# Kernel tuning notes

Measured on AMD Instinct MI355X. Metric: run time of the kernel, lower is better.

The kernel has to match this reference:

```python
import jax, jax.numpy as jnp
import numpy as np

N, E, B = 100000, 400000, 4096      # nodes, directed edges, graphs
P, d = 4, 49                        # phm_dim, per-component dim; D = P*d = 196
L = 3                               # message-passing layers
D1, D2 = 64, 32                     # downstream per-component dims (256/4, 128/4)


def setup_inputs():
    key = jax.random.key(0)
    ks = jax.random.split(key, 20)
    def nrm(k, shape, s=0.1):
        return jax.random.normal(k, shape, dtype=jnp.float32) * s
    return {
        "x": jax.random.randint(ks[0], (N, 9), 0, 119),
        "edge_index": jax.random.randint(ks[1], (2, E), 0, N),
        "edge_attr": jax.random.randint(ks[2], (E, 3), 0, 8),
        "batch": jnp.sort(jax.random.randint(ks[3], (N,), 0, B)),
        # encoders: summed categorical embeddings in hypercomplex form [*, P, d]
        "atom_emb": nrm(ks[4], (9, 119, P, d)),
        "bond_emb": nrm(ks[5], (L, 3, 8, P, d)),
        # per-layer PHM conv: contribution matrices A (phm rule) + component weights W
        "conv_A": nrm(ks[6], (L, P, P, P), 0.5),
        "conv_W": nrm(ks[7], (L, P, d, d)),
        "conv_b": jnp.zeros((L, P, d), jnp.float32),
        "mp_gamma": jnp.ones((L, P * d), jnp.float32),
        "mp_beta": jnp.zeros((L, P * d), jnp.float32),
        # soft-attention pooling: PHM linear + real transformer gate
        "pool_A": nrm(ks[8], (P, P, P), 0.5),
        "pool_W": nrm(ks[9], (P, d, d)),
        "pool_b": jnp.zeros((P, d), jnp.float32),
        "pool_rt_w": nrm(ks[10], (P,), 0.5),
        "pool_rt_b": jnp.zeros((d,), jnp.float32),
        # downstream PHM MLP 196 -> 256 -> 128 -> 4*1, then real trafo -> 1
        "dn_A": nrm(ks[11], (3, P, P, P), 0.5),
        "dn1_W": nrm(ks[12], (P, d, D1)),
        "dn1_b": jnp.zeros((P, D1), jnp.float32),
        "dn1_gamma": jnp.ones((P * D1,), jnp.float32),
        "dn1_beta": jnp.zeros((P * D1,), jnp.float32),
        "dn2_W": nrm(ks[13], (P, D1, D2)),
        "dn2_b": jnp.zeros((P, D2), jnp.float32),
        "dn2_gamma": jnp.ones((P * D2,), jnp.float32),
        "dn2_beta": jnp.zeros((P * D2,), jnp.float32),
        "dn3_W": nrm(ks[14], (P, D2, 1)),
        "dn3_b": jnp.zeros((P, 1), jnp.float32),
        "rt_w": nrm(ks[15], (P,), 0.5),
        "rt_b": jnp.zeros((1,), jnp.float32),
    }


def phm_linear(x, A, W, b):
    # PHM linear: y = x @ (sum_i kron(A_i, W_i)) + b, on [n, P, din] -> [n, P, dout]
    return jnp.einsum('nkp,ikj,ipq->njq', x, A, W) + b


def naive_bn(x, gamma, beta, eps=1e-5):
    # naive batch norm over the batch axis, per flattened hypercomplex feature
    n, p, dd = x.shape
    x2 = x.reshape(n, p * dd)
    mu = x2.mean(axis=0)
    var = x2.var(axis=0)
    x2 = (x2 - mu) * jax.lax.rsqrt(var + eps) * gamma + beta
    return x2.reshape(n, p, dd)


def reference(x, edge_index, edge_attr, batch, atom_emb, bond_emb,
              conv_A, conv_W, conv_b, mp_gamma, mp_beta,
              pool_A, pool_W, pool_b, pool_rt_w, pool_rt_b,
              dn_A, dn1_W, dn1_b, dn1_gamma, dn1_beta,
              dn2_W, dn2_b, dn2_gamma, dn2_beta, dn3_W, dn3_b, rt_w, rt_b):
    src, dst = edge_index[0], edge_index[1]
    # atom encoder: sum embeddings of 9 categorical features -> [N, P, d]
    h0 = atom_emb[jnp.arange(9), x].sum(axis=1)
    h = h0
    for l in range(L):  # small fixed layer count
        # bond encoder for this layer -> [E, P, d]
        e = bond_emb[l][jnp.arange(3), edge_attr].sum(axis=1)
        # message = x_j + e_ij (identity msg encoder); self-loop (zero edge feat) adds h
        m = h[src] + e
        agg = jax.ops.segment_sum(m, dst, num_segments=N) + h
        z = phm_linear(agg, conv_A[l], conv_W[l], conv_b[l])
        z = jax.nn.relu(naive_bn(z, mp_gamma[l], mp_beta[l]))
        h = z + h0  # skip-connect to first embedding (sc_type='first')
    # soft-attention pooling: real-valued sigmoid gate per node feature
    g = jax.nn.sigmoid(
        jnp.einsum('npk,p->nk', phm_linear(h, pool_A, pool_W, pool_b), pool_rt_w)
        + pool_rt_b)
    pooled = jax.ops.segment_sum(h * g[:, None, :], batch, num_segments=B)  # [B, P, d]
    # downstream PHM MLP with naive batch norm + relu
    z = jax.nn.relu(naive_bn(phm_linear(pooled, dn_A[0], dn1_W, dn1_b), dn1_gamma, dn1_beta))
    z = jax.nn.relu(naive_bn(phm_linear(z, dn_A[1], dn2_W, dn2_b), dn2_gamma, dn2_beta))
    o = phm_linear(z, dn_A[2], dn3_W, dn3_b)          # [B, P, 1]
    return jnp.einsum('npk,p->nk', o, rt_w) + rt_b    # [B, 1]
```

## Files before the change

kernel.cpp:

```cpp
#include <hip/hip_runtime.h>
#include <cstdint>
#include <cstddef>

#define N_NODES 100000
#define N_EDGES 400000
#define N_GRAPHS 4096
#define DF 196
#define DD 49
#define NPB 5
#define TST 200
#define WSLOT 14336
#define EST 232

typedef __bf16 bf16x8 __attribute__((ext_vector_type(8)));
typedef float f32x4 __attribute__((ext_vector_type(4)));

__device__ __forceinline__ unsigned short f2bf(float f) {
  unsigned int u = __float_as_uint(f);
  u = u + 0x7FFFu + ((u >> 16) & 1u);
  return (unsigned short)(u >> 16);
}
__device__ __forceinline__ float bf2f(unsigned short h) {
  return __uint_as_float(((unsigned int)h) << 16);
}

__global__ void convert_wfrag_kernel(const float* __restrict__ cA,
                                     const float* __restrict__ cW,
                                     unsigned short* __restrict__ wfrag) {
  int idx = blockIdx.x * blockDim.x + threadIdx.x;
  if (idx >= 3 * 100352) return;
  int l = idx / 100352;
  int r = idx - l * 100352;
  int ct = r / 7168; int r1 = r - ct * 7168;
  int ks = r1 / 1024; int r2 = r1 - ks * 1024;
  int h = r2 / 512;  int r3 = r2 - h * 512;
  int ln = r3 / 8;   int j = r3 - ln * 8;
  int col = ct * 16 + (ln & 15);
  int k = ks * 32 + (ln >> 4) * 8 + j;
  float v = 0.f;
  if (col < DF && k < DF) {
    int k4 = k / DD, p = k - (k / DD) * DD;
    int j4 = col / DD, q = col - (col / DD) * DD;
#pragma unroll
    for (int i = 0; i < 4; i++)
      v += cA[((l * 4 + i) * 4 + k4) * 4 + j4] * cW[((l * 4 + i) * DD + p) * DD + q];
  }
  unsigned short hi = f2bf(v);
  wfrag[idx] = (h == 0) ? hi : f2bf(v - bf2f(hi));
}

__global__ void setup_small_kernel(const float* __restrict__ bond, float* __restrict__ lut,
                                   const float* __restrict__ pA, const float* __restrict__ pW,
                                   const float* __restrict__ pb, const float* __restrict__ rtw,
                                   const float* __restrict__ rtb,
                                   float* __restrict__ gateW, float* __restrict__ gbias,
                                   const float* __restrict__ dnA,
                                   const float* __restrict__ W1, const float* __restrict__ W2,
                                   const float* __restrict__ W3,
                                   float* __restrict__ M1, float* __restrict__ M2,
                                   float* __restrict__ M3) {
  int idx0 = blockIdx.x * blockDim.x + threadIdx.x;
  const int NL = 3 * 512 * DF;
  const int NG = DF * DD + DD;
  const int n1 = DF * 256, n2 = 256 * 128, n3 = 128 * 4;
  if (idx0 < NL) {
    int idx = idx0;
    int l = idx / (512 * DF);
    int r = idx - l * (512 * DF);
    int code = r / DF, c = r - (r / DF) * DF;
    int a0 = code & 7, a1 = (code >> 3) & 7, a2 = (code >> 6) & 7;
    lut[idx] = bond[((l * 3 + 0) * 8 + a0) * DF + c]
             + bond[((l * 3 + 1) * 8 + a1) * DF + c]
             + bond[((l * 3 + 2) * 8 + a2) * DF + c];
  } else if (idx0 < NL + NG) {
    int idx = idx0 - NL;
    if (idx < DF * DD) {
      int r = idx / DD, q = idx - (idx / DD) * DD;
      int k = r / DD, p = r - (r / DD) * DD;
      float s = 0.f;
#pragma unroll
      for (int i = 0; i < 4; i++) {
        float aw = 0.f;
#pragma unroll
        for (int j = 0; j < 4; j++) aw += pA[(i * 4 + k) * 4 + j] * rtw[j];
        s += aw * pW[(i * DD + p) * DD + q];
      }
      gateW[idx] = s;
    } else {
      int q = idx - DF * DD;
      float s = rtb[q];
#pragma unroll
      for (int j = 0; j < 4; j++) s += rtw[j] * pb[j * DD + q];
      gbias[q] = s;
    }
  } else if (idx0 < NL + NG + n1 + n2 + n3) {
    int idx = idx0 - NL - NG;
    if (idx < n1) {
      int r = idx >> 8, c = idx & 255;
      int k = r / DD, p = r - (r / DD) * DD;
      int j = c >> 6, Q = c & 63;
      float s = 0.f;
#pragma unroll
      for (int i = 0; i < 4; i++) s += dnA[i * 16 + k * 4 + j] * W1[(i * DD + p) * 64 + Q];
      M1[idx] = s;
    } else if (idx < n1 + n2) {
      int m = idx - n1;
      int r = m >> 7, c = m & 127;
      int k = r >> 6, p = r & 63, j = c >> 5, q = c & 31;
      float s = 0.f;
#pragma unroll
      for (int i = 0; i < 4; i++) s += dnA[64 + i * 16 + k * 4 + j] * W2[(i * 64 + p) * 32 + q];
      M2[m] = s;
    } else {
      int m = idx - n1 - n2;
      int r = m >> 2, j = m & 3;
      int k = r >> 5, p = r & 31;
      float s = 0.f;
#pragma unroll
      for (int i = 0; i < 4; i++) s += dnA[128 + i * 16 + k * 4 + j] * W3[i * 32 + p];
      M3[m] = s;
    }
  }
}

__global__ void hist_kernel(const int* __restrict__ dst, int* __restrict__ counts) {
  int e = blockIdx.x * blockDim.x + threadIdx.x;
  if (e < N_EDGES) atomicAdd(&counts[dst[e]], 1);
}

__global__ void scan_local_kernel(const int* __restrict__ counts, int* __restrict__ offs,
                                  int* __restrict__ bsum) {
  __shared__ int sm[256];
  int tid = threadIdx.x;
  int gid = blockIdx.x * 256 + tid;
  int v = (gid < N_NODES) ? counts[gid] : 0;
  sm[tid] = v;
  __syncthreads();
  for (int d = 1; d < 256; d <<= 1) {
    int add = (tid >= d) ? sm[tid - d] : 0;
    __syncthreads();
    sm[tid] += add;
    __syncthreads();
  }
  if (gid < N_NODES) offs[gid] = sm[tid] - v;
  if (tid == 255) bsum[blockIdx.x] = sm[255];
}

__global__ void scan_bsum_kernel(int* __restrict__ bsum, int* __restrict__ bpre, int nb) {
  __shared__ int sm[512];
  int tid = threadIdx.x;
  int v = (tid < nb) ? bsum[tid] : 0;
  sm[tid] = v;
  __syncthreads();
  for (int d = 1; d < 512; d <<= 1) {
    int add = (tid >= d) ? sm[tid - d] : 0;
    __syncthreads();
    sm[tid] += add;
    __syncthreads();
  }
  if (tid < nb) bpre[tid] = sm[tid] - v;
}

__global__ void add_off_kernel(int* __restrict__ offs, const int* __restrict__ bpre) {
  int gid = blockIdx.x * blockDim.x + threadIdx.x;
  if (gid < N_NODES) offs[gid] += bpre[gid >> 8];
  if (gid == 0) offs[N_NODES] = N_EDGES;
}

__global__ void scatter_kernel(const int* __restrict__ src, const int* __restrict__ dst,
                               const int* __restrict__ ea, int* __restrict__ counts,
                               const int* __restrict__ offs,
                               unsigned int* __restrict__ sorted) {
  int e = blockIdx.x * blockDim.x + threadIdx.x;
  if (e >= N_EDGES) return;
  int d = dst[e];
  int code = ea[e * 3 + 0] | (ea[e * 3 + 1] << 3) | (ea[e * 3 + 2] << 6);
  int pos = offs[d] + atomicSub(&counts[d], 1) - 1;
  sorted[pos] = (unsigned int)src[e] | ((unsigned int)code << 17);
}

__global__ void sortseg_kernel(const int* __restrict__ offs,
                               unsigned int* __restrict__ sorted) {
  int n = blockIdx.x * blockDim.x + threadIdx.x;
  if (n >= N_NODES) return;
  int s = offs[n], e = offs[n + 1];
  for (int i = s + 1; i < e; i++) {
    unsigned int v = sorted[i];
    int j = i - 1;
    while (j >= s && sorted[j] > v) { sorted[j + 1] = sorted[j]; j--; }
    sorted[j + 1] = v;
  }
}

__global__ void atom_enc_kernel(const int* __restrict__ x, const float* __restrict__ emb,
                                float* __restrict__ h0) {
  int idx = blockIdx.x * blockDim.x + threadIdx.x;
  if (idx >= N_NODES * DF) return;
  int n = idx / DF;
  int c = idx - n * DF;
  float s = 0.f;
#pragma unroll
  for (int f = 0; f < 9; f++) {
    int xi = x[n * 9 + f];
    s += emb[(f * 119 + xi) * DF + c];
  }
  h0[idx] = s;
}

__global__ __launch_bounds__(256)
void agg_kernel(const float* __restrict__ h, const int* __restrict__ offs,
                const unsigned int* __restrict__ sorted, const float* __restrict__ lut,
                unsigned short* __restrict__ tH, unsigned short* __restrict__ tL) {
  int t = threadIdx.x;
  int i = t / 49, q = t - i * 49;
  if (i >= NPB) return;
  int node = blockIdx.x * NPB + i;
  if (node >= N_NODES) return;
  const float4* h4 = (const float4*)h;
  const float4* l4 = (const float4*)lut;
  float4 acc = h4[(size_t)node * 49 + q];
  int s = offs[node], e = offs[node + 1];
  for (int k = s; k < e; k++) {
    unsigned int se = sorted[k];
    int srcn = se & 0x1FFFF;
    int code = se >> 17;
    float4 hv = h4[(size_t)srcn * 49 + q];
    float4 lv = l4[(size_t)code * 49 + q];
    acc.x += hv.x + lv.x;
    acc.y += hv.y + lv.y;
    acc.z += hv.z + lv.z;
    acc.w += hv.w + lv.w;
  }
  ushort4 hh, ll;
  hh.x = f2bf(acc.x); ll.x = f2bf(acc.x - bf2f(hh.x));
  hh.y = f2bf(acc.y); ll.y = f2bf(acc.y - bf2f(hh.y));
  hh.z = f2bf(acc.z); ll.z = f2bf(acc.z - bf2f(hh.z));
  hh.w = f2bf(acc.w); ll.w = f2bf(acc.w - bf2f(hh.w));
  size_t ob = (size_t)node * TST + q * 4;
  *(ushort4*)(tH + ob) = hh;
  *(ushort4*)(tL + ob) = ll;
  if (q == 48) {
    ushort4 z = make_ushort4(0, 0, 0, 0);
    *(ushort4*)(tH + (size_t)node * TST + 196) = z;
    *(ushort4*)(tL + (size_t)node * TST + 196) = z;
  }
}

__global__ __launch_bounds__(256, 2)
void conv_mfma_kernel(unsigned short* __restrict__ tH,
                      unsigned short* __restrict__ tL,
                      const unsigned short* __restrict__ wfrag,
                      const float* __restrict__ bias,
                      float* __restrict__ stats) {
  __shared__ __align__(16) unsigned short smW[2 * 64 * EST];
  const int t = threadIdx.x;
  const int lane = t & 63;
  const int w = t >> 6;
  const int li = lane & 15;
  const int rg = lane >> 4;
  const int rowbase = blockIdx.x * 128 + w * 32;

  f32x4 acc[2][14];
#pragma unroll
  for (int rt = 0; rt < 2; rt++)
#pragma unroll
    for (int ct = 0; ct < 14; ct++) acc[rt][ct] = (f32x4){0.f, 0.f, 0.f, 0.f};

  uint4 b0h[2], b0l[2], b1h[2], b1l[2], b2h[2], b2l[2];
  uint4 wr0[7], wr1[7];

#define LOADA(ks, aH, aL)                                                      \
  {                                                                            \
    _Pragma("unroll") for (int rt = 0; rt < 2; rt++) {                         \
      size_t o = (size_t)(rowbase + rt * 16 + li) * TST + (ks) * 32 + rg * 8;  \
      aH[rt] = *(const uint4*)(tH + o);                                        \
      aL[rt] = *(const uint4*)(tL + o);                                        \
    }                                                                          \
  }

#define GLOADW(ks, wr)                                                         \
  {                                                                            \
    _Pragma("unroll") for (int f0 = 0; f0 < 7; f0++) {                         \
      int f = f0 * 256 + t;                                                    \
      int ln = f & 63, g = f >> 6;                                             \
      int hh = g & 1, ct = g >> 1;                                             \
      wr[f0] = *(const uint4*)(wfrag +                                         \
          (((size_t)(ct * 7 + (ks)) * 2 + hh) * 512 + ln * 8));                \
    }                                                                          \
  }

#define DSWRITEW(wr, sbase)                                                    \
  {                                                                            \
    _Pragma("unroll") for (int f0 = 0; f0 < 7; f0++) {                         \
      int f = f0 * 256 + t;                                                    \
      int ln = f & 63, g = f >> 6;                                             \
      int hh = g & 1, ct = g >> 1;                                             \
      *(uint4*)(smW + (sbase) + ((ct * 2 + hh) * 512 + ln * 8)) = wr[f0];      \
    }                                                                          \
  }

#define COMPUTE(sbase, aH, aL)                                                 \
  {                                                                            \
    _Pragma("unroll") for (int ct = 0; ct < 14; ct++) {                        \
      bf16x8 bh = *(const bf16x8*)(smW + (sbase) + ((ct * 2 + 0) * 512 + lane * 8)); \
      bf16x8 bl = *(const bf16x8*)(smW + (sbase) + ((ct * 2 + 1) * 512 + lane * 8)); \
      _Pragma("unroll") for (int rt = 0; rt < 2; rt++) {                       \
        bf16x8 ah = *(const bf16x8*)&aH[rt];                                   \
        bf16x8 al = *(const bf16x8*)&aL[rt];                                   \
        acc[rt][ct] = __builtin_amdgcn_mfma_f32_16x16x32_bf16(ah, bh, acc[rt][ct], 0, 0, 0); \
        acc[rt][ct] = __builtin_amdgcn_mfma_f32_16x16x32_bf16(al, bh, acc[rt][ct], 0, 0, 0); \
        acc[rt][ct] = __builtin_amdgcn_mfma_f32_16x16x32_bf16(ah, bl, acc[rt][ct], 0, 0, 0); \
      }                                                                        \
    }                                                                          \
  }

  GLOADW(0, wr0);
  GLOADW(1, wr1);
  LOADA(0, b0h, b0l);
  LOADA(1, b1h, b1l);
  LOADA(2, b2h, b2l);
  DSWRITEW(wr0, 0);
  GLOADW(2, wr0);
  __syncthreads();
  COMPUTE(0, b0h, b0l);
  DSWRITEW(wr1, WSLOT);
  GLOADW(3, wr1);
  LOADA(3, b0h, b0l);
  __syncthreads();
  COMPUTE(WSLOT, b1h, b1l);
  DSWRITEW(wr0, 0);
  GLOADW(4, wr0);
  LOADA(4, b1h, b1l);
  __syncthreads();
  COMPUTE(0, b2h, b2l);
  DSWRITEW(wr1, WSLOT);
  GLOADW(5, wr1);
  LOADA(5, b2h, b2l);
  __syncthreads();
  COMPUTE(WSLOT, b0h, b0l);
  DSWRITEW(wr0, 0);
  GLOADW(6, wr0);
  LOADA(6, b0h, b0l);
  __syncthreads();
  COMPUTE(0, b1h, b1l);
  DSWRITEW(wr1, WSLOT);
  __syncthreads();
  COMPUTE(WSLOT, b2h, b2l);
  DSWRITEW(wr0, 0);
  __syncthreads();
  COMPUTE(0, b0h, b0l);

  float part[14], psq[14];
#pragma unroll
  for (int ct = 0; ct < 14; ct++) { part[ct] = 0.f; psq[ct] = 0.f; }

  unsigned short* lhi = smW;
  unsigned short* llo = smW + 64 * EST;

#pragma unroll
  for (int half = 0; half < 2; half++) {
    __syncthreads();
    if ((w >> 1) == half) {
      int rl0 = (w & 1) * 32;
#pragma unroll
      for (int ct = 0; ct < 14; ct++) {
        int c = ct * 16 + li;
        float bv = (c < DF) ? bias[c] : 0.f;
#pragma unroll
        for (int rt = 0; rt < 2; rt++) {
#pragma unroll
          for (int r = 0; r < 4; r++) {
            int row = rl0 + rt * 16 + rg * 4 + r;
            int gr = rowbase + rt * 16 + rg * 4 + r;
            float y = acc[rt][ct][r] + bv;
            if (gr < N_NODES && c < DF) { part[ct] += y; psq[ct] += y * y; }
            unsigned short hi = f2bf(y);
            lhi[row * EST + c] = hi;
            llo[row * EST + c] = f2bf(y - bf2f(hi));
          }
        }
      }
    }
    __syncthreads();
    for (int idx = t; idx < 1600; idx += 256) {
      int row = idx / 25, u = idx - (idx / 25) * 25;
      int gr = blockIdx.x * 128 + half * 64 + row;
      if (gr < N_NODES) {
        uint4 vh = *(const uint4*)(lhi + row * EST + u * 8);
        uint4 vl = *(const uint4*)(llo + row * EST + u * 8);
        if (u == 24) { vh.z = 0u; vh.w = 0u; vl.z = 0u; vl.w = 0u; }
        *(uint4*)(tH + (size_t)gr * TST + u * 8) = vh;
        *(uint4*)(tL + (size_t)gr * TST + u * 8) = vl;
      }
    }
  }

  __syncthreads();
  float* redS = (float*)smW;
  float* redQ = redS + 4 * 224;
#pragma unroll
  for (int ct = 0; ct < 14; ct++) {
    float p = part[ct], q = psq[ct];
    p += __shfl_xor(p, 16, 64); p += __shfl_xor(p, 32, 64);
    q += __shfl_xor(q, 16, 64); q += __shfl_xor(q, 32, 64);
    if (rg == 0) { redS[w * 224 + ct * 16 + li] = p; redQ[w * 224 + ct * 16 + li] = q; }
  }
  __syncthreads();
  if (t < DF) {
    float s1 = redS[t] + redS[224 + t] + redS[448 + t] + redS[672 + t];
    float s2 = redQ[t] + redQ[224 + t] + redQ[448 + t] + redQ[672 + t];
    atomicAdd(&stats[t], s1);
    atomicAdd(&stats[DF + t], s2);
  }
#undef LOADA
#undef GLOADW
#undef DSWRITEW
#undef COMPUTE
}

__global__ void bn_relu_split_kernel(const unsigned short* __restrict__ tH,
                                     const unsigned short* __restrict__ tL,
                                     const float* __restrict__ stats,
                                     const float* __restrict__ gamma,
                                     const float* __restrict__ beta,
                                     const float* __restrict__ h0,
                                     float* __restrict__ h) {
  int idx = blockIdx.x * blockDim.x + threadIdx.x;
  if (idx >= N_NODES * DD) return;
  int n = idx / DD, q = idx - (idx / DD) * DD;
  size_t ib = (size_t)n * TST + q * 4;
  ushort4 hv = *(const ushort4*)(tH + ib);
  ushort4 lv = *(const ushort4*)(tL + ib);
  size_t fb = (size_t)n * DF + q * 4;
  float4 sk = *(const float4*)(h0 + fb);
  int c = q * 4;
  const float invN = 1.f / N_NODES;
  float4 o;
  {
    float z = bf2f(hv.x) + bf2f(lv.x);
    float mu = stats[c + 0] * invN;
    float var = stats[DF + c + 0] * invN - mu * mu;
    o.x = fmaxf((z - mu) * rsqrtf(var + 1e-5f) * gamma[c + 0] + beta[c + 0], 0.f) + sk.x;
  }
  {
    float z = bf2f(hv.y) + bf2f(lv.y);
    float mu = stats[c + 1] * invN;
    float var = stats[DF + c + 1] * invN - mu * mu;
    o.y = fmaxf((z - mu) * rsqrtf(var + 1e-5f) * gamma[c + 1] + beta[c + 1], 0.f) + sk.y;
  }
  {
    float z = bf2f(hv.z) + bf2f(lv.z);
    float mu = stats[c + 2] * invN;
    float var = stats[DF + c + 2] * invN - mu * mu;
    o.z = fmaxf((z - mu) * rsqrtf(var + 1e-5f) * gamma[c + 2] + beta[c + 2], 0.f) + sk.z;
  }
  {
    float z = bf2f(hv.w) + bf2f(lv.w);
    float mu = stats[c + 3] * invN;
    float var = stats[DF + c + 3] * invN - mu * mu;
    o.w = fmaxf((z - mu) * rsqrtf(var + 1e-5f) * gamma[c + 3] + beta[c + 3], 0.f) + sk.w;
  }
  *(float4*)(h + fb) = o;
}

template<int S, int MODE>
__launch_bounds__(256)
__global__ void gemm_kernel(const float* X, const float* __restrict__ W,
                            const float* __restrict__ bias, float* Y,
                            float* __restrict__ stats, int Nrows, int K, int NC) {
  constexpr int WN = S * 64;
  __shared__ __align__(16) float At[32][64];
  __shared__ __align__(16) float Wl[32][WN];
  const int t = threadIdx.x;
  const int tx = t & 15;
  const int ty = t >> 4;
  const int r0 = blockIdx.x * 64;

  float acc[S][4][4];
#pragma unroll
  for (int s = 0; s < S; s++)
#pragma unroll
    for (int i = 0; i < 4; i++)
#pragma unroll
      for (int j = 0; j < 4; j++) acc[s][i][j] = 0.f;

  const int lr = t >> 2;
  const int kb = (t & 3) * 8;
  constexpr int TPR = S * 16;
  const int cw = (t % TPR) * 4;
  const int kr = t / TPR;
  constexpr int RPP = 256 / TPR;
  constexpr int PASSES = 32 / RPP;

  for (int k0 = 0; k0 < K; k0 += 32) {
    {
      const int gr = r0 + lr;
      const float* xp = X + (size_t)gr * K + k0 + kb;
      if (gr < Nrows && (k0 + kb + 7) < K) {
        float4 v0 = *(const float4*)(xp);
        float4 v1 = *(const float4*)(xp + 4);
        At[kb + 0][lr] = v0.x; At[kb + 1][lr] = v0.y;
        At[kb + 2][lr] = v0.z; At[kb + 3][lr] = v0.w;
        At[kb + 4][lr] = v1.x; At[kb + 5][lr] = v1.y;
        At[kb + 6][lr] = v1.z; At[kb + 7][lr] = v1.w;
      } else {
#pragma unroll
        for (int i = 0; i < 8; i++) {
          int kk = kb + i;
          float v = 0.f;
          if (gr < Nrows && (k0 + kk) < K) v = xp[i];
          At[kk][lr] = v;
        }
      }
    }
#pragma unroll
    for (int ps = 0; ps < PASSES; ps++) {
      int kk = kr + ps * RPP;
      int gk = k0 + kk;
      if (gk < K && (cw + 3) < NC && ((NC & 3) == 0)) {
        float4 v = *(const float4*)(W + (size_t)gk * NC + cw);
        Wl[kk][cw + 0] = v.x; Wl[kk][cw + 1] = v.y;
        Wl[kk][cw + 2] = v.z; Wl[kk][cw + 3] = v.w;
      } else {
#pragma unroll
        for (int j = 0; j < 4; j++) {
          int c = cw + j;
          float v = 0.f;
          if (gk < K && c < NC) v = W[(size_t)gk * NC + c];
          Wl[kk][c] = v;
        }
      }
    }
    __syncthreads();
#pragma unroll 4
    for (int kk = 0; kk < 32; kk++) {
      float4 a = *(const float4*)&At[kk][ty * 4];
      float av[4] = {a.x, a.y, a.z, a.w};
#pragma unroll
      for (int s = 0; s < S; s++) {
        float4 w = *(const float4*)&Wl[kk][s * 64 + tx * 4];
        float wv[4] = {w.x, w.y, w.z, w.w};
#pragma unroll
        for (int i = 0; i < 4; i++)
#pragma unroll
          for (int j = 0; j < 4; j++)
            acc[s][i][j] = fmaf(av[i], wv[j], acc[s][i][j]);
      }
    }
    __syncthreads();
  }

#pragma unroll
  for (int s = 0; s < S; s++)
#pragma unroll
    for (int j = 0; j < 4; j++) {
      int c = s * 64 + tx * 4 + j;
      float bv = (c < NC) ? bias[c] : 0.f;
#pragma unroll
      for (int i = 0; i < 4; i++) {
        float y = acc[s][i][j] + bv;
        if (MODE == 1) y = 1.f / (1.f + __expf(-y));
        acc[s][i][j] = y;
      }
    }
#pragma unroll
  for (int i = 0; i < 4; i++) {
    int gr = r0 + ty * 4 + i;
    if (gr < Nrows) {
#pragma unroll
      for (int s = 0; s < S; s++)
#pragma unroll
        for (int j = 0; j < 4; j++) {
          int c = s * 64 + tx * 4 + j;
          if (c < NC) Y[(size_t)gr * NC + c] = acc[s][i][j];
        }
    }
  }
  if (MODE == 0) {
    float* red = &Wl[0][0];
    __syncthreads();
#pragma unroll
    for (int s = 0; s < S; s++)
#pragma unroll
      for (int j = 0; j < 4; j++) {
        float p = 0.f;
#pragma unroll
        for (int i = 0; i < 4; i++)
          if ((r0 + ty * 4 + i) < Nrows) p += acc[s][i][j];
        red[ty * WN + s * 64 + tx * 4 + j] = p;
      }
    __syncthreads();
    if (t < WN) {
      float tot = 0.f;
#pragma unroll
      for (int yy = 0; yy < 16; yy++) tot += red[yy * WN + t];
      if (t < NC) atomicAdd(&stats[t], tot);
    }
    __syncthreads();
#pragma unroll
    for (int s = 0; s < S; s++)
#pragma unroll
      for (int j = 0; j < 4; j++) {
        float p = 0.f;
#pragma unroll
        for (int i = 0; i < 4; i++)
          if ((r0 + ty * 4 + i) < Nrows) p += acc[s][i][j] * acc[s][i][j];
        red[ty * WN + s * 64 + tx * 4 + j] = p;
      }
    __syncthreads();
    if (t < WN) {
      float tot = 0.f;
#pragma unroll
      for (int yy = 0; yy < 16; yy++) tot += red[yy * WN + t];
      if (t < NC) atomicAdd(&stats[NC + t], tot);
    }
  }
}

__global__ void bn_relu_kernel(const float* __restrict__ z, const float* __restrict__ stats,
                               const float* __restrict__ gamma, const float* __restrict__ beta,
                               float* __restrict__ out,
                               int total, int NC, float invN) {
  int idx = blockIdx.x * blockDim.x + threadIdx.x;
  if (idx >= total) return;
  int c = idx % NC;
  float mu = stats[c] * invN;
  float var = stats[NC + c] * invN - mu * mu;
  float v = (z[idx] - mu) * rsqrtf(var + 1e-5f) * gamma[c] + beta[c];
  out[idx] = fmaxf(v, 0.f);
}

__device__ __forceinline__ int lower_bound_dev(const int* a, int n, int v) {
  int lo = 0, hi = n;
  while (lo < hi) { int mid = (lo + hi) >> 1; if (a[mid] < v) lo = mid + 1; else hi = mid; }
  return lo;
}

__global__ void pool_kernel(const float* __restrict__ h, const float* __restrict__ g,
                            const int* __restrict__ batch, float* __restrict__ pooled) {
  int b = blockIdx.x;
  __shared__ int bounds[2];
  if (threadIdx.x == 0) {
    bounds[0] = lower_bound_dev(batch, N_NODES, b);
    bounds[1] = lower_bound_dev(batch, N_NODES, b + 1);
  }
  __syncthreads();
  int c = threadIdx.x;
  if (c >= DF) return;
  int s = bounds[0], e = bounds[1];
  int q = c % DD;
  float acc = 0.f;
  for (int n = s; n < e; n++)
    acc = fmaf(h[(size_t)n * DF + c], g[(size_t)n * DD + q], acc);
  pooled[(size_t)b * DF + c] = acc;
}

__global__ void final_kernel(const float* __restrict__ z2, const float* __restrict__ M3,
                             const float* __restrict__ b3, const float* __restrict__ rtw,
                             const float* __restrict__ rtb, float* __restrict__ out) {
  __shared__ float sM[128 * 4];
  __shared__ float srw[4];
  __shared__ float srb;
  int t = threadIdx.x;
  for (int i = t; i < 512; i += 256) sM[i] = M3[i];
  if (t < 4) srw[t] = rtw[t];
  if (t == 4) srb = rtb[0];
  __syncthreads();
  int b = blockIdx.x * blockDim.x + t;
  if (b >= N_GRAPHS) return;
  float o0 = b3[0], o1 = b3[1], o2 = b3[2], o3 = b3[3];
  const float* zp = z2 + (size_t)b * 128;
  for (int p = 0; p < 128; p++) {
    float v = zp[p];
    o0 = fmaf(v, sM[p * 4 + 0], o0);
    o1 = fmaf(v, sM[p * 4 + 1], o1);
    o2 = fmaf(v, sM[p * 4 + 2], o2);
    o3 = fmaf(v, sM[p * 4 + 3], o3);
  }
  out[b] = srb + o0 * srw[0] + o1 * srw[1] + o2 * srw[2] + o3 * srw[3];
}

extern "C" void kernel_launch(void* const* d_in, const int* in_sizes, int n_in,
                              void* d_out, int out_size, void* d_ws, size_t ws_size,
                              hipStream_t stream) {
  (void)in_sizes; (void)n_in; (void)out_size; (void)ws_size;
  const int* x          = (const int*)d_in[0];
  const int* edge_index = (const int*)d_in[1];
  const int* edge_attr  = (const int*)d_in[2];
  const int* batch      = (const int*)d_in[3];
  const float* atom_emb = (const float*)d_in[4];
  const float* bond_emb = (const float*)d_in[5];
  const float* conv_A   = (const float*)d_in[6];
  const float* conv_W   = (const float*)d_in[7];
  const float* conv_b   = (const float*)d_in[8];
  const float* mp_gamma = (const float*)d_in[9];
  const float* mp_beta  = (const float*)d_in[10];
  const float* pool_A   = (const float*)d_in[11];
  const float* pool_W   = (const float*)d_in[12];
  const float* pool_b   = (const float*)d_in[13];
  const float* pool_rt_w = (const float*)d_in[14];
  const float* pool_rt_b = (const float*)d_in[15];
  const float* dn_A     = (const float*)d_in[16];
  const float* dn1_W    = (const float*)d_in[17];
  const float* dn1_b    = (const float*)d_in[18];
  const float* dn1_gamma = (const float*)d_in[19];
  const float* dn1_beta = (const float*)d_in[20];
  const float* dn2_W    = (const float*)d_in[21];
  const float* dn2_b    = (const float*)d_in[22];
  const float* dn2_gamma = (const float*)d_in[23];
  const float* dn2_beta = (const float*)d_in[24];
  const float* dn3_W    = (const float*)d_in[25];
  const float* dn3_b    = (const float*)d_in[26];
  const float* rt_w     = (const float*)d_in[27];
  const float* rt_b     = (const float*)d_in[28];
  float* out = (float*)d_out;

  char* ws = (char*)d_ws;
  size_t off = 0;
  auto alloc = [&](size_t bytes) -> char* {
    char* p = ws + off;
    off = (off + bytes + 255) & ~(size_t)255;
    return p;
  };
  const size_t HBYTES = (size_t)N_NODES * DF * sizeof(float);
  float* h0 = (float*)alloc(HBYTES);
  float* h  = (float*)alloc(HBYTES);
  unsigned short* tH = (unsigned short*)alloc((size_t)N_NODES * TST * 2 + 4096);
  unsigned short* tL = (unsigned short*)alloc((size_t)N_NODES * TST * 2 + 4096);
  float* g      = (float*)tH;
  float* pooled = (float*)((char*)tH + (((size_t)N_NODES * DD * 4 + 255) & ~(size_t)255));
  float* z1     = (float*)((char*)pooled + (((size_t)N_GRAPHS * DF * 4 + 255) & ~(size_t)255));
  float* z2     = (float*)((char*)z1 + (((size_t)N_GRAPHS * 256 * 4 + 255) & ~(size_t)255));
  unsigned short* wfrag = (unsigned short*)alloc((size_t)3 * 100352 * 2);
  float* gateW  = (float*)alloc(DF * DD * 4);
  float* gbias  = (float*)alloc(64 * 4);
  float* M1     = (float*)alloc(DF * 256 * 4);
  float* M2     = (float*)alloc(256 * 128 * 4);
  float* M3     = (float*)alloc(128 * 4 * 4);
  float* stats  = (float*)alloc(2048 * 4);
  int*  counts  = (int*)alloc(N_NODES * 4);
  int*  offs    = (int*)alloc((N_NODES + 1) * 4);
  unsigned int* sorted = (unsigned int*)alloc((size_t)N_EDGES * 4);
  float* lut    = (float*)alloc((size_t)3 * 512 * DF * 4);
  int*  bsum    = (int*)alloc(512 * 4);
  int*  bpre    = (int*)alloc(512 * 4);

  const int* src = edge_index;
  const int* dst = edge_index + N_EDGES;
  const int NB = (N_NODES + 255) / 256;

  hipMemsetAsync(stats, 0, 2048 * 4, stream);
  hipMemsetAsync(counts, 0, N_NODES * 4, stream);

  convert_wfrag_kernel<<<(3 * 100352 + 255) / 256, 256, 0, stream>>>(conv_A, conv_W, wfrag);
  {
    const int total = 3 * 512 * DF + (DF * DD + DD) + (DF * 256 + 256 * 128 + 128 * 4);
    setup_small_kernel<<<(total + 255) / 256, 256, 0, stream>>>(
        bond_emb, lut, pool_A, pool_W, pool_b, pool_rt_w, pool_rt_b, gateW, gbias,
        dn_A, dn1_W, dn2_W, dn3_W, M1, M2, M3);
  }

  hist_kernel<<<(N_EDGES + 255) / 256, 256, 0, stream>>>(dst, counts);
  scan_local_kernel<<<NB, 256, 0, stream>>>(counts, offs, bsum);
  scan_bsum_kernel<<<1, 512, 0, stream>>>(bsum, bpre, NB);
  add_off_kernel<<<NB, 256, 0, stream>>>(offs, bpre);
  scatter_kernel<<<(N_EDGES + 255) / 256, 256, 0, stream>>>(
      src, dst, edge_attr, counts, offs, sorted);
  sortseg_kernel<<<NB, 256, 0, stream>>>(offs, sorted);

  atom_enc_kernel<<<(N_NODES * DF + 255) / 256, 256, 0, stream>>>(x, atom_emb, h0);

  const int NCONV = (N_NODES + 127) / 128;
  for (int l = 0; l < 3; l++) {
    const float* hl = (l == 0) ? h0 : h;
    agg_kernel<<<(N_NODES + NPB - 1) / NPB, 256, 0, stream>>>(
        hl, offs, sorted, lut + (size_t)l * 512 * DF, tH, tL);
    float* st = stats + l * 392;
    conv_mfma_kernel<<<NCONV, 256, 0, stream>>>(
        tH, tL, wfrag + (size_t)l * 100352, conv_b + (size_t)l * DF, st);
    bn_relu_split_kernel<<<(N_NODES * DD + 255) / 256, 256, 0, stream>>>(
        tH, tL, st, mp_gamma + l * DF, mp_beta + l * DF, h0, h);
  }

  gemm_kernel<1, 1><<<(N_NODES + 63) / 64, 256, 0, stream>>>(
      h, gateW, gbias, g, nullptr, N_NODES, DF, DD);
  pool_kernel<<<N_GRAPHS, 256, 0, stream>>>(h, g, batch, pooled);

  gemm_kernel<4, 0><<<(N_GRAPHS + 63) / 64, 256, 0, stream>>>(
      pooled, M1, dn1_b, z1, stats + 1176, N_GRAPHS, DF, 256);
  bn_relu_kernel<<<(N_GRAPHS * 256 + 255) / 256, 256, 0, stream>>>(
      z1, stats + 1176, dn1_gamma, dn1_beta, z1, N_GRAPHS * 256, 256, 1.f / N_GRAPHS);
  gemm_kernel<2, 0><<<(N_GRAPHS + 63) / 64, 256, 0, stream>>>(
      z1, M2, dn2_b, z2, stats + 1688, N_GRAPHS, 256, 128);
  bn_relu_kernel<<<(N_GRAPHS * 128 + 255) / 256, 256, 0, stream>>>(
      z2, stats + 1688, dn2_gamma, dn2_beta, z2, N_GRAPHS * 128, 128, 1.f / N_GRAPHS);
  final_kernel<<<(N_GRAPHS + 255) / 256, 256, 0, stream>>>(z2, M3, dn3_b, rt_w, rt_b, out);
}
```

Before: 1.011 ms.

## Stream weight fragments directly to LDS with global_load_lds and deepen A prefetch

Replaces the register-staged weight path (global load into VGPRs, then ds_write) with direct global-to-LDS loads through __builtin_amdgcn_global_load_lds. The double-buffered pipeline is restructured so each stage issues the next weight slab and the A-fragment prefetch before its MFMA compute, and a fourth A buffer is added. This is meant to free the 14 uint4 weight registers and remove the LDS write instructions. The risk is ordering: the direct loads need vmcnt waits before the barrier, and the compiler may not insert them correctly.

```diff
diff --git a/kernel.cpp b/kernel.cpp
--- a/kernel.cpp
+++ b/kernel.cpp
@@ -11,6 +11,9 @@
 #define TST 200
 #define WSLOT 14336
 #define EST 232
+
+#define AS1 __attribute__((address_space(1)))
+#define AS3 __attribute__((address_space(3)))
 
 typedef __bf16 bf16x8 __attribute__((ext_vector_type(8)));
 typedef float f32x4 __attribute__((ext_vector_type(4)));
@@ -266,8 +269,7 @@
 #pragma unroll
     for (int ct = 0; ct < 14; ct++) acc[rt][ct] = (f32x4){0.f, 0.f, 0.f, 0.f};
 
-  uint4 b0h[2], b0l[2], b1h[2], b1l[2], b2h[2], b2l[2];
-  uint4 wr0[7], wr1[7];
+  uint4 b0h[2], b0l[2], b1h[2], b1l[2], b2h[2], b2l[2], b3h[2], b3l[2];
 
 #define LOADA(ks, aH, aL)                                                      \
   {                                                                            \
@@ -278,24 +280,14 @@
     }                                                                          \
   }
 
-#define GLOADW(ks, wr)                                                         \
+#define WLOAD(ks, sbase)                                                       \
   {                                                                            \
     _Pragma("unroll") for (int f0 = 0; f0 < 7; f0++) {                         \
-      int f = f0 * 256 + t;                                                    \
-      int ln = f & 63, g = f >> 6;                                             \
+      int g = f0 * 4 + w;                                                      \
       int hh = g & 1, ct = g >> 1;                                             \
-      wr[f0] = *(const uint4*)(wfrag +                                         \
-          (((size_t)(ct * 7 + (ks)) * 2 + hh) * 512 + ln * 8));                \
-    }                                                                          \
-  }
-
-#define DSWRITEW(wr, sbase)                                                    \
-  {                                                                            \
-    _Pragma("unroll") for (int f0 = 0; f0 < 7; f0++) {                         \
-      int f = f0 * 256 + t;                                                    \
-      int ln = f & 63, g = f >> 6;                                             \
-      int hh = g & 1, ct = g >> 1;                                             \
-      *(uint4*)(smW + (sbase) + ((ct * 2 + hh) * 512 + ln * 8)) = wr[f0];      \
+      __builtin_amdgcn_global_load_lds(                                        \
+          (AS1 const void*)(wfrag + ((size_t)(ct * 7 + (ks)) * 2 + hh) * 512 + lane * 8), \
+          (AS3 void*)(smW + (sbase) + (ct * 2 + hh) * 512), 16, 0, 0);         \
     }                                                                          \
   }
 
@@ -314,41 +306,24 @@
     }                                                                          \
   }
 
-  GLOADW(0, wr0);
-  GLOADW(1, wr1);
+  WLOAD(0, 0);
   LOADA(0, b0h, b0l);
   LOADA(1, b1h, b1l);
   LOADA(2, b2h, b2l);
-  DSWRITEW(wr0, 0);
-  GLOADW(2, wr0);
-  __syncthreads();
-  COMPUTE(0, b0h, b0l);
-  DSWRITEW(wr1, WSLOT);
-  GLOADW(3, wr1);
-  LOADA(3, b0h, b0l);
-  __syncthreads();
-  COMPUTE(WSLOT, b1h, b1l);
-  DSWRITEW(wr0, 0);
-  GLOADW(4, wr0);
-  LOADA(4, b1h, b1l);
+  __syncthreads();
+  WLOAD(1, WSLOT); LOADA(3, b3h, b3l); COMPUTE(0, b0h, b0l);
+  __syncthreads();
+  WLOAD(2, 0);     LOADA(4, b0h, b0l); COMPUTE(WSLOT, b1h, b1l);
+  __syncthreads();
+  WLOAD(3, WSLOT); LOADA(5, b1h, b1l); COMPUTE(0, b2h, b2l);
+  __syncthreads();
+  WLOAD(4, 0);     LOADA(6, b2h, b2l); COMPUTE(WSLOT, b3h, b3l);
+  __syncthreads();
+  WLOAD(5, WSLOT);                     COMPUTE(0, b0h, b0l);
+  __syncthreads();
+  WLOAD(6, 0);                         COMPUTE(WSLOT, b1h, b1l);
   __syncthreads();
   COMPUTE(0, b2h, b2l);
-  DSWRITEW(wr1, WSLOT);
-  GLOADW(5, wr1);
-  LOADA(5, b2h, b2l);
-  __syncthreads();
-  COMPUTE(WSLOT, b0h, b0l);
-  DSWRITEW(wr0, 0);
-  GLOADW(6, wr0);
-  LOADA(6, b0h, b0l);
-  __syncthreads();
-  COMPUTE(0, b1h, b1l);
-  DSWRITEW(wr1, WSLOT);
-  __syncthreads();
-  COMPUTE(WSLOT, b2h, b2l);
-  DSWRITEW(wr0, 0);
-  __syncthreads();
-  COMPUTE(0, b0h, b0l);
 
   float part[14], psq[14];
 #pragma unroll
@@ -413,8 +388,7 @@
     atomicAdd(&stats[DF + t], s2);
   }
 #undef LOADA
-#undef GLOADW
-#undef DSWRITEW
+#undef WLOAD
 #undef COMPUTE
 }
 
```

After: 891.7 us. 11.8% less time.
